# Optimization experiments

Hardware: AMD Instinct MI355X
Metric: run time of the kernel (lower is better)

Reference implementation:

```python
import jax, jax.numpy as jnp
import numpy as np

D = 128
N = 300000
M = 262144
LN_EPS = 1e-5


def setup_inputs() -> dict:
    key = jax.random.key(0)
    ks = jax.random.split(key, 20)
    inp = {
        'h_p': jax.random.normal(ks[0], (N, D), jnp.float32),
        'h_k': jax.random.normal(ks[1], (N, D), jnp.float32),
        'h_o': jax.random.normal(ks[2], (M, D), jnp.float32),
        'weight_o': jax.random.normal(ks[3], (D, D // 2), jnp.float32) * 0.15,
        'weight_p': jax.random.normal(ks[4], (D, D // 2), jnp.float32) * 0.15,
        'lin_W': jax.random.normal(ks[5], (D, D), jnp.float32) * 0.08,
        'lin_b': jax.random.normal(ks[6], (D,), jnp.float32) * 0.05,
        'bias': jax.random.normal(ks[7], (D,), jnp.float32) * 0.05,
        'Wq': jax.random.normal(ks[8], (D, D), jnp.float32) * 0.08,
        'bq': jax.random.normal(ks[9], (D,), jnp.float32) * 0.05,
        'Wk': jax.random.normal(ks[10], (D, D), jnp.float32) * 0.08,
        'bk': jax.random.normal(ks[11], (D,), jnp.float32) * 0.05,
        'Wv': jax.random.normal(ks[12], (D, D), jnp.float32) * 0.08,
        'bv': jax.random.normal(ks[13], (D,), jnp.float32) * 0.05,
        'W1': jax.random.normal(ks[14], (D, D), jnp.float32) * 0.08,
        'b1': jax.random.normal(ks[15], (D,), jnp.float32) * 0.05,
        'ln_g': jnp.ones((D,), jnp.float32),
        'ln_b': jnp.zeros((D,), jnp.float32),
        'mutual_index_p': jax.random.randint(ks[16], (M,), 0, N, jnp.int32),
        'mutual_index_k': jax.random.randint(ks[17], (M,), 0, N, jnp.int32),
        'propagation_node_num': N,
        'knowledge_node_num': N,
    }
    return inp


def reference(h_p, h_k, h_o, weight_o, weight_p, lin_W, lin_b, bias,
              Wq, bq, Wk, bk, Wv, bv, W1, b1, ln_g, ln_b,
              mutual_index_p, mutual_index_k,
              propagation_node_num, knowledge_node_num):
    # gather: Q from h_o rows, K from paired h_p/h_k rows (seq len 2)
    ho_sel = h_o[mutual_index_p]                       # [M, D]
    q = ho_sel[:, None, :]                             # [M, 1, D]
    k_in = jnp.stack([h_p[mutual_index_p], h_k[mutual_index_k]], axis=1)  # [M, 2, D]

    Q = q @ Wq.T + bq                                  # [M, 1, D]
    K = k_in @ Wk.T + bk                               # [M, 2, D]
    V = k_in @ Wv.T + bv                               # [M, 2, D]

    scale = jnp.float32(D) ** -0.5
    attn = jax.nn.softmax(jnp.einsum('mqd,mkd->mqk', Q, K) * scale, axis=-1)  # [M,1,2]
    ctx = jnp.einsum('mqk,mkd->mqd', attn, V)          # [M, 1, D]

    fusion = ctx @ W1.T + b1                           # dropout is identity in eval
    mu = jnp.mean(fusion, axis=-1, keepdims=True)
    var = jnp.var(fusion, axis=-1, keepdims=True)
    fusion = (fusion - mu) * jax.lax.rsqrt(var + LN_EPS) * ln_g + ln_b
    fusion = fusion[:, 0, :]                           # [M, D]

    trans_ho = ho_sel @ weight_o                       # [M, D/2]
    trans_pk = fusion @ weight_p                       # [M, D/2]
    out = jnp.tanh(jnp.concatenate([trans_ho, trans_pk], axis=1))
    out = jax.nn.leaky_relu(out @ lin_W.T + lin_b, negative_slope=0.01)
    out = out + bias                                   # [M, D]

    h_p = h_p.at[mutual_index_p].set(out)
    h_k = h_k.at[mutual_index_k].set(out)
    return (h_p, h_k)
```

## Files before the change

### kernel.cpp

```cpp
#include <hip/hip_runtime.h>
#include <stdint.h>

#define D 128
#define NROWS 300000
#define MIDX 262144
#define SBH 132
#define WAVE_BUF (16 * SBH)

typedef __attribute__((ext_vector_type(8))) short short8_t;
typedef __attribute__((ext_vector_type(4))) short short4_t;
typedef __attribute__((ext_vector_type(4))) float float4v;

__device__ __forceinline__ short f2bf(float x) {
  uint32_t u = __float_as_uint(x);
  u = (u + 0x7FFFu + ((u >> 16) & 1u)) >> 16;
  return (short)u;
}

__global__ void winners_kernel(const int* __restrict__ idx_p,
                               const int* __restrict__ idx_k,
                               int* __restrict__ wp, int* __restrict__ wk) {
  int m = blockIdx.x * 256 + threadIdx.x;
  if (m < MIDX) {
    atomicMax(&wp[idx_p[m]], m);
    atomicMax(&wk[idx_k[m]], m);
  }
}

__global__ __launch_bounds__(256)
void copyrest_kernel(const float* __restrict__ h_p, const float* __restrict__ h_k,
                     const int* __restrict__ wp, const int* __restrict__ wk,
                     float* __restrict__ out_p, float* __restrict__ out_k) {
  int g = blockIdx.x * 256 + threadIdx.x;
  int row = g >> 5;
  if (row >= NROWS) return;
  int c = (g & 31) << 2;
  size_t off = (size_t)row * D + c;
  if (wp[row] < 0) *(float4v*)(out_p + off) = *(const float4v*)(h_p + off);
  if (wk[row] < 0) *(float4v*)(out_k + off) = *(const float4v*)(h_k + off);
}

__global__ void pack_kernel(const float* __restrict__ Wq, const float* __restrict__ Wk,
                            const float* __restrict__ Wv, const float* __restrict__ W1,
                            const float* __restrict__ Wl, const float* __restrict__ Wo,
                            const float* __restrict__ Wp, short* __restrict__ dst) {
  int slot = blockIdx.x;
  int lane = threadIdx.x;
  const float* W; int base; int trans; int rel;
  if      (slot < 32)  { W = Wq; base = 0;     trans = 1; rel = slot; }
  else if (slot < 64)  { W = Wk; base = 16384; trans = 1; rel = slot - 32; }
  else if (slot < 96)  { W = Wv; base = 32768; trans = 1; rel = slot - 64; }
  else if (slot < 128) { W = W1; base = 49152; trans = 1; rel = slot - 96; }
  else if (slot < 160) { W = Wl; base = 65536; trans = 1; rel = slot - 128; }
  else if (slot < 176) { W = Wo; base = 81920; trans = 0; rel = slot - 160; }
  else                 { W = Wp; base = 90112; trans = 0; rel = slot - 176; }
  int t = rel >> 2, s = rel & 3;
  int n = 16 * t + (lane & 15);
  int kb = 32 * s + 8 * (lane >> 4);
  short* o = dst + base + (size_t)(rel * 64 + lane) * 8;
  #pragma unroll
  for (int j = 0; j < 8; j++) {
    float v = trans ? W[n * 128 + kb + j] : W[(kb + j) * 64 + n];
    o[j] = f2bf(v);
  }
}

__device__ __forceinline__ float4v gemm_tile_lds(const short8_t a[4], const short* B,
                                                 int t, int lane) {
  float4v acc = {0.f, 0.f, 0.f, 0.f};
  #pragma unroll
  for (int s = 0; s < 4; s++) {
    short8_t b = *(const short8_t*)(B + ((t * 4 + s) * 64 + lane) * 8);
    acc = __builtin_amdgcn_mfma_f32_16x16x32_bf16(a[s], b, acc, 0, 0, 0);
  }
  return acc;
}

__device__ __forceinline__ void load_row_frags(const float* __restrict__ row, int q, short8_t out[4]) {
  #pragma unroll
  for (int s = 0; s < 4; s++) {
    float4v v0 = *(const float4v*)(row + 32 * s + 8 * q);
    float4v v1 = *(const float4v*)(row + 32 * s + 8 * q + 4);
    short8_t r;
    r[0] = f2bf(v0[0]); r[1] = f2bf(v0[1]); r[2] = f2bf(v0[2]); r[3] = f2bf(v0[3]);
    r[4] = f2bf(v1[0]); r[5] = f2bf(v1[1]); r[6] = f2bf(v1[2]); r[7] = f2bf(v1[3]);
    out[s] = r;
  }
}

__device__ __forceinline__ void read_a_frags(const short* sb, int l15, int q, short8_t out[4]) {
  #pragma unroll
  for (int s = 0; s < 4; s++) {
    const short* p = sb + l15 * SBH + 32 * s + 8 * q;
    short4_t lo = *(const short4_t*)p;
    short4_t hi = *(const short4_t*)(p + 4);
    short8_t v;
    v[0] = lo[0]; v[1] = lo[1]; v[2] = lo[2]; v[3] = lo[3];
    v[4] = hi[0]; v[5] = hi[1]; v[6] = hi[2]; v[7] = hi[3];
    out[s] = v;
  }
}

__device__ __forceinline__ float red16(float v) {
  v += __shfl_xor(v, 1);
  v += __shfl_xor(v, 2);
  v += __shfl_xor(v, 4);
  v += __shfl_xor(v, 8);
  return v;
}

__global__ __launch_bounds__(256, 2)
void fused_kernel(const float* __restrict__ h_p, const float* __restrict__ h_k,
                  const float* __restrict__ h_o, int ho_rows,
                  const int* __restrict__ idx_p, const int* __restrict__ idx_k,
                  const short* __restrict__ wbuf,
                  const float* __restrict__ bq, const float* __restrict__ bk,
                  const float* __restrict__ bv, const float* __restrict__ b1,
                  const float* __restrict__ linb, const float* __restrict__ bias,
                  const float* __restrict__ lng, const float* __restrict__ lnb,
                  const int* __restrict__ wp, const int* __restrict__ wk,
                  float* __restrict__ out_p, float* __restrict__ out_k)
{
  const short* Bq_ = wbuf;
  const short* Bk_ = wbuf + 16384;
  const short* Bv_ = wbuf + 32768;
  const short* B1_ = wbuf + 49152;
  const short* Bl_ = wbuf + 65536;
  const short* Bo_ = wbuf + 81920;

  __shared__ short bsh[16384];
  __shared__ float smem[4 * WAVE_BUF];

  const int tid  = threadIdx.x;
  const int wave = tid >> 6;
  const int lane = tid & 63;
  const int l15  = lane & 15;
  const int q    = lane >> 4;

  float* fbuf = smem + wave * WAVE_BUF;
  short* sbuf = (short*)fbuf;

  const int m0   = blockIdx.x * 64 + wave * 16;
  const int mrow = m0 + l15;
  const int ip = idx_p[mrow];
  const int ik = idx_k[mrow];
  const int ipo = (ip < ho_rows) ? ip : (ho_rows - 1);

  short8_t aho[4], ahp[4], ahk[4];
  load_row_frags(h_o + (size_t)ipo * D, q, aho);
  load_row_frags(h_p + (size_t)ip * D, q, ahp);
  load_row_frags(h_k + (size_t)ik * D, q, ahk);

  short8_t breg[8];

  #define LDSTAGE(SRC) { _Pragma("unroll") \
    for (int r_ = 0; r_ < 8; r_++) breg[r_] = *(const short8_t*)((SRC) + (r_ * 256 + tid) * 8); }
  #define STSTAGE() { _Pragma("unroll") \
    for (int r_ = 0; r_ < 8; r_++) *(short8_t*)(bsh + (r_ * 256 + tid) * 8) = breg[r_]; }

  LDSTAGE(Bq_);
  STSTAGE();
  LDSTAGE(Bk_);
  __syncthreads();

  float4v Q[8];
  #pragma unroll
  for (int t = 0; t < 8; t++) {
    Q[t] = gemm_tile_lds(aho, bsh, t, lane) + bq[16 * t + l15];
  }

  __syncthreads();
  STSTAGE();
  LDSTAGE(Bv_);
  __syncthreads();

  float4v p0 = {0,0,0,0}, p1 = {0,0,0,0};
  #pragma unroll
  for (int t = 0; t < 8; t++) {
    float bkv = bk[16 * t + l15];
    float4v k0 = gemm_tile_lds(ahp, bsh, t, lane) + bkv;
    float4v k1 = gemm_tile_lds(ahk, bsh, t, lane) + bkv;
    p0 += Q[t] * k0;
    p1 += Q[t] * k1;
  }
  float a0[4], a1[4];
  #pragma unroll
  for (int r = 0; r < 4; r++) {
    float s0 = red16(p0[r]) * 0.08838834764831845f;
    float s1 = red16(p1[r]) * 0.08838834764831845f;
    float mx = fmaxf(s0, s1);
    float e0 = __expf(s0 - mx), e1 = __expf(s1 - mx);
    float inv = 1.0f / (e0 + e1);
    a0[r] = e0 * inv;
    a1[r] = e1 * inv;
  }

  __syncthreads();
  STSTAGE();
  LDSTAGE(B1_);
  __syncthreads();

  float4v ctx[8];
  #pragma unroll
  for (int t = 0; t < 8; t++) {
    float bvv = bv[16 * t + l15];
    float4v v0 = gemm_tile_lds(ahp, bsh, t, lane) + bvv;
    float4v v1 = gemm_tile_lds(ahk, bsh, t, lane) + bvv;
    float4v c;
    #pragma unroll
    for (int r = 0; r < 4; r++) c[r] = a0[r] * v0[r] + a1[r] * v1[r];
    ctx[t] = c;
  }

  #pragma unroll
  for (int t = 0; t < 8; t++)
    #pragma unroll
    for (int r = 0; r < 4; r++)
      sbuf[(4 * q + r) * SBH + 16 * t + l15] = f2bf(ctx[t][r]);
  short8_t afu[4];
  read_a_frags(sbuf, l15, q, afu);

  __syncthreads();
  STSTAGE();
  LDSTAGE(Bo_);
  __syncthreads();

  float4v F[8];
  float4v sum = {0,0,0,0}, ssq = {0,0,0,0};
  #pragma unroll
  for (int t = 0; t < 8; t++) {
    float4v f = gemm_tile_lds(afu, bsh, t, lane) + b1[16 * t + l15];
    F[t] = f;
    sum += f;
    ssq += f * f;
  }
  #pragma unroll
  for (int r = 0; r < 4; r++) {
    float s  = red16(sum[r]);
    float s2 = red16(ssq[r]);
    float mu  = s * (1.0f / 128.0f);
    float var = s2 * (1.0f / 128.0f) - mu * mu;
    float rs  = rsqrtf(var + 1e-5f);
    #pragma unroll
    for (int t = 0; t < 8; t++) F[t][r] = (F[t][r] - mu) * rs;
  }
  #pragma unroll
  for (int t = 0; t < 8; t++) {
    int col = 16 * t + l15;
    float g = lng[col], b = lnb[col];
    #pragma unroll
    for (int r = 0; r < 4; r++)
      sbuf[(4 * q + r) * SBH + col] = f2bf(F[t][r] * g + b);
  }
  short8_t afn[4];
  read_a_frags(sbuf, l15, q, afn);

  __syncthreads();
  STSTAGE();
  LDSTAGE(Bl_);
  __syncthreads();

  float4v U[8];
  #pragma unroll
  for (int t = 0; t < 4; t++) U[t]     = gemm_tile_lds(aho, bsh, t, lane);
  #pragma unroll
  for (int t = 0; t < 4; t++) U[4 + t] = gemm_tile_lds(afn, bsh + 8192, t, lane);
  #pragma unroll
  for (int t = 0; t < 8; t++) {
    #pragma unroll
    for (int r = 0; r < 4; r++) {
      float x  = U[t][r];
      float e  = __expf(-2.0f * fabsf(x));
      float th = (1.0f - e) / (1.0f + e);
      sbuf[(4 * q + r) * SBH + 16 * t + l15] = f2bf(copysignf(th, x));
    }
  }
  short8_t au[4];
  read_a_frags(sbuf, l15, q, au);

  __syncthreads();
  STSTAGE();
  __syncthreads();

  #pragma unroll
  for (int t = 0; t < 8; t++) {
    int col = 16 * t + l15;
    float4v z = gemm_tile_lds(au, bsh, t, lane) + linb[col];
    float bb = bias[col];
    #pragma unroll
    for (int r = 0; r < 4; r++) {
      float x = z[r];
      x = (x > 0.0f) ? x : 0.01f * x;
      fbuf[(4 * q + r) * SBH + col] = x + bb;
    }
  }

  int r_out = lane >> 2;
  int cb    = (lane & 3) * 32;
  int mg    = m0 + r_out;
  int ip2 = idx_p[mg];
  int ik2 = idx_k[mg];
  bool dop = (wp[ip2] == mg);
  bool dok = (wk[ik2] == mg);
  const float* src = fbuf + r_out * SBH + cb;
  float* dp = out_p + (size_t)ip2 * D + cb;
  float* dk = out_k + (size_t)ik2 * D + cb;
  #pragma unroll
  for (int c = 0; c < 32; c += 4) {
    float4v v = *(const float4v*)(src + c);
    if (dop) *(float4v*)(dp + c) = v;
    if (dok) *(float4v*)(dk + c) = v;
  }
  #undef LDSTAGE
  #undef STSTAGE
}

extern "C" void kernel_launch(void* const* d_in, const int* in_sizes, int n_in,
                              void* d_out, int out_size, void* d_ws, size_t ws_size,
                              hipStream_t stream) {
  const float* h_p      = (const float*)d_in[0];
  const float* h_k      = (const float*)d_in[1];
  const float* h_o      = (const float*)d_in[2];
  const float* weight_o = (const float*)d_in[3];
  const float* weight_p = (const float*)d_in[4];
  const float* lin_W    = (const float*)d_in[5];
  const float* lin_b    = (const float*)d_in[6];
  const float* bias     = (const float*)d_in[7];
  const float* Wq       = (const float*)d_in[8];
  const float* bq       = (const float*)d_in[9];
  const float* Wk       = (const float*)d_in[10];
  const float* bk       = (const float*)d_in[11];
  const float* Wv       = (const float*)d_in[12];
  const float* bv       = (const float*)d_in[13];
  const float* W1       = (const float*)d_in[14];
  const float* b1       = (const float*)d_in[15];
  const float* ln_g     = (const float*)d_in[16];
  const float* ln_b     = (const float*)d_in[17];
  const int*   idx_p    = (const int*)d_in[18];
  const int*   idx_k    = (const int*)d_in[19];

  const int ho_rows = in_sizes[2] / D;

  float* out_p = (float*)d_out;
  float* out_k = out_p + (size_t)NROWS * D;

  int* wp = (int*)d_ws;
  int* wk = wp + NROWS;
  short* wbuf = (short*)((char*)d_ws + (size_t)2 * NROWS * 4);

  hipMemsetAsync(wp, 0xFF, (size_t)2 * NROWS * sizeof(int), stream);

  winners_kernel<<<dim3(MIDX / 256), dim3(256), 0, stream>>>(idx_p, idx_k, wp, wk);
  copyrest_kernel<<<dim3((NROWS * 32 + 255) / 256), dim3(256), 0, stream>>>(
      h_p, h_k, wp, wk, out_p, out_k);
  pack_kernel<<<dim3(192), dim3(64), 0, stream>>>(Wq, Wk, Wv, W1, lin_W, weight_o, weight_p, wbuf);
  fused_kernel<<<dim3(MIDX / 64), dim3(256), 0, stream>>>(
      h_p, h_k, h_o, ho_rows, idx_p, idx_k, wbuf, bq, bk, bv, b1, lin_b, bias, ln_g, ln_b,
      wp, wk, out_p, out_k);
}
```

Baseline: 763.0 us.

## Fold Wq and Wk into one matrix and process two row tiles per wave

Measured after the change: 750.9 us. No clear change (-1.6%).

```diff
diff --git a/kernel.cpp b/kernel.cpp
--- a/kernel.cpp
+++ b/kernel.cpp
@@ -5,7 +5,7 @@
 #define NROWS 300000
 #define MIDX 262144
 #define SBH 132
-#define WAVE_BUF (16 * SBH)
+#define WBUF_SH (32 * SBH)
 
 typedef __attribute__((ext_vector_type(8))) short short8_t;
 typedef __attribute__((ext_vector_type(4))) short short4_t;
@@ -15,6 +15,9 @@
   uint32_t u = __float_as_uint(x);
   u = (u + 0x7FFFu + ((u >> 16) & 1u)) >> 16;
   return (short)u;
+}
+__device__ __forceinline__ float bf2f(short s) {
+  return __uint_as_float(((uint32_t)(uint16_t)s) << 16);
 }
 
 __global__ void winners_kernel(const int* __restrict__ idx_p,
@@ -40,40 +43,70 @@
   if (wk[row] < 0) *(float4v*)(out_k + off) = *(const float4v*)(h_k + off);
 }
 
-__global__ void pack_kernel(const float* __restrict__ Wq, const float* __restrict__ Wk,
-                            const float* __restrict__ Wv, const float* __restrict__ W1,
-                            const float* __restrict__ Wl, const float* __restrict__ Wo,
-                            const float* __restrict__ Wp, short* __restrict__ dst) {
+__global__ void prep_m_kernel(const float* __restrict__ Wq, const float* __restrict__ Wk,
+                              const float* __restrict__ bq,
+                              float* __restrict__ Mbuf, float* __restrict__ v2) {
+  int b = blockIdx.x;
+  if (b < 64) {
+    int d = ((b >> 3) << 4) + (threadIdx.x >> 4);
+    int e = ((b & 7) << 4) + (threadIdx.x & 15);
+    float acc = 0.f;
+    for (int j = 0; j < 128; j++) acc += Wq[j * 128 + d] * Wk[j * 128 + e];
+    Mbuf[d * 128 + e] = acc;
+  } else if (threadIdx.x < 128) {
+    int e = threadIdx.x;
+    float acc = 0.f;
+    for (int j = 0; j < 128; j++) acc += bq[j] * Wk[j * 128 + e];
+    v2[e] = acc;
+  }
+}
+
+__global__ void pack_kernel(const float* __restrict__ Mb, const float* __restrict__ Wv,
+                            const float* __restrict__ W1, const float* __restrict__ Wl,
+                            const float* __restrict__ Wo, const float* __restrict__ Wp,
+                            short* __restrict__ dst) {
   int slot = blockIdx.x;
   int lane = threadIdx.x;
-  const float* W; int base; int trans; int rel;
-  if      (slot < 32)  { W = Wq; base = 0;     trans = 1; rel = slot; }
-  else if (slot < 64)  { W = Wk; base = 16384; trans = 1; rel = slot - 32; }
-  else if (slot < 96)  { W = Wv; base = 32768; trans = 1; rel = slot - 64; }
-  else if (slot < 128) { W = W1; base = 49152; trans = 1; rel = slot - 96; }
-  else if (slot < 160) { W = Wl; base = 65536; trans = 1; rel = slot - 128; }
-  else if (slot < 176) { W = Wo; base = 81920; trans = 0; rel = slot - 160; }
-  else                 { W = Wp; base = 90112; trans = 0; rel = slot - 176; }
+  const float* W; int base; int trans; int rel; int wdt = 128;
+  if      (slot < 32)  { W = Mb; base = 0;     trans = 0; rel = slot; }
+  else if (slot < 64)  { W = Wv; base = 16384; trans = 1; rel = slot - 32; }
+  else if (slot < 96)  { W = W1; base = 32768; trans = 1; rel = slot - 64; }
+  else if (slot < 112) { W = Wo; base = 49152; trans = 0; rel = slot - 96;  wdt = 64; }
+  else if (slot < 128) { W = Wp; base = 57344; trans = 0; rel = slot - 112; wdt = 64; }
+  else                 { W = Wl; base = 65536; trans = 1; rel = slot - 128; }
   int t = rel >> 2, s = rel & 3;
   int n = 16 * t + (lane & 15);
   int kb = 32 * s + 8 * (lane >> 4);
   short* o = dst + base + (size_t)(rel * 64 + lane) * 8;
   #pragma unroll
   for (int j = 0; j < 8; j++) {
-    float v = trans ? W[n * 128 + kb + j] : W[(kb + j) * 64 + n];
+    float v = trans ? W[n * 128 + kb + j] : W[(kb + j) * wdt + n];
     o[j] = f2bf(v);
   }
 }
 
-__device__ __forceinline__ float4v gemm_tile_lds(const short8_t a[4], const short* B,
-                                                 int t, int lane) {
-  float4v acc = {0.f, 0.f, 0.f, 0.f};
+__device__ __forceinline__ void gemm2(const short8_t a0[4], const short8_t a1[4],
+                                      const short* B, int t, int lane,
+                                      float4v& c0, float4v& c1) {
   #pragma unroll
   for (int s = 0; s < 4; s++) {
     short8_t b = *(const short8_t*)(B + ((t * 4 + s) * 64 + lane) * 8);
-    acc = __builtin_amdgcn_mfma_f32_16x16x32_bf16(a[s], b, acc, 0, 0, 0);
-  }
-  return acc;
+    c0 = __builtin_amdgcn_mfma_f32_16x16x32_bf16(a0[s], b, c0, 0, 0, 0);
+    c1 = __builtin_amdgcn_mfma_f32_16x16x32_bf16(a1[s], b, c1, 0, 0, 0);
+  }
+}
+__device__ __forceinline__ void gemm4(const short8_t a0[4], const short8_t a1[4],
+                                      const short8_t a2[4], const short8_t a3[4],
+                                      const short* B, int t, int lane,
+                                      float4v& c0, float4v& c1, float4v& c2, float4v& c3) {
+  #pragma unroll
+  for (int s = 0; s < 4; s++) {
+    short8_t b = *(const short8_t*)(B + ((t * 4 + s) * 64 + lane) * 8);
+    c0 = __builtin_amdgcn_mfma_f32_16x16x32_bf16(a0[s], b, c0, 0, 0, 0);
+    c1 = __builtin_amdgcn_mfma_f32_16x16x32_bf16(a1[s], b, c1, 0, 0, 0);
+    c2 = __builtin_amdgcn_mfma_f32_16x16x32_bf16(a2[s], b, c2, 0, 0, 0);
+    c3 = __builtin_amdgcn_mfma_f32_16x16x32_bf16(a3[s], b, c3, 0, 0, 0);
+  }
 }
 
 __device__ __forceinline__ void load_row_frags(const float* __restrict__ row, int q, short8_t out[4]) {
@@ -88,10 +121,10 @@
   }
 }
 
-__device__ __forceinline__ void read_a_frags(const short* sb, int l15, int q, short8_t out[4]) {
+__device__ __forceinline__ void read_a_frags(const short* sb, int row, int q, short8_t out[4]) {
   #pragma unroll
   for (int s = 0; s < 4; s++) {
-    const short* p = sb + l15 * SBH + 32 * s + 8 * q;
+    const short* p = sb + row * SBH + 32 * s + 8 * q;
     short4_t lo = *(const short4_t*)p;
     short4_t hi = *(const short4_t*)(p + 4);
     short8_t v;
@@ -113,23 +146,21 @@
 void fused_kernel(const float* __restrict__ h_p, const float* __restrict__ h_k,
                   const float* __restrict__ h_o, int ho_rows,
                   const int* __restrict__ idx_p, const int* __restrict__ idx_k,
-                  const short* __restrict__ wbuf,
-                  const float* __restrict__ bq, const float* __restrict__ bk,
+                  const short* __restrict__ wbuf, const float* __restrict__ v2,
                   const float* __restrict__ bv, const float* __restrict__ b1,
                   const float* __restrict__ linb, const float* __restrict__ bias,
                   const float* __restrict__ lng, const float* __restrict__ lnb,
                   const int* __restrict__ wp, const int* __restrict__ wk,
                   float* __restrict__ out_p, float* __restrict__ out_k)
 {
-  const short* Bq_ = wbuf;
-  const short* Bk_ = wbuf + 16384;
-  const short* Bv_ = wbuf + 32768;
-  const short* B1_ = wbuf + 49152;
-  const short* Bl_ = wbuf + 65536;
-  const short* Bo_ = wbuf + 81920;
+  const short* Bm_  = wbuf;
+  const short* Bv_  = wbuf + 16384;
+  const short* B1_  = wbuf + 32768;
+  const short* Bop_ = wbuf + 49152;
+  const short* Bl_  = wbuf + 65536;
 
   __shared__ short bsh[16384];
-  __shared__ float smem[4 * WAVE_BUF];
+  __shared__ short tmem[4 * WBUF_SH];
 
   const int tid  = threadIdx.x;
   const int wave = tid >> 6;
@@ -137,19 +168,24 @@
   const int l15  = lane & 15;
   const int q    = lane >> 4;
 
-  float* fbuf = smem + wave * WAVE_BUF;
-  short* sbuf = (short*)fbuf;
-
-  const int m0   = blockIdx.x * 64 + wave * 16;
-  const int mrow = m0 + l15;
-  const int ip = idx_p[mrow];
-  const int ik = idx_k[mrow];
-  const int ipo = (ip < ho_rows) ? ip : (ho_rows - 1);
-
-  short8_t aho[4], ahp[4], ahk[4];
-  load_row_frags(h_o + (size_t)ipo * D, q, aho);
-  load_row_frags(h_p + (size_t)ip * D, q, ahp);
-  load_row_frags(h_k + (size_t)ik * D, q, ahk);
+  short* sbuf = tmem + wave * WBUF_SH;
+  float* fbuf = (float*)sbuf;
+
+  const int m0  = blockIdx.x * 128 + wave * 32;
+  const int mr0 = m0 + l15;
+  const int mr1 = m0 + 16 + l15;
+  const int ip0 = idx_p[mr0], ik0 = idx_k[mr0];
+  const int ip1 = idx_p[mr1], ik1 = idx_k[mr1];
+  const int ipo0 = (ip0 < ho_rows) ? ip0 : (ho_rows - 1);
+  const int ipo1 = (ip1 < ho_rows) ? ip1 : (ho_rows - 1);
+
+  short8_t aho0[4], ahp0[4], ahk0[4], aho1[4], ahp1[4], ahk1[4];
+  load_row_frags(h_o + (size_t)ipo0 * D, q, aho0);
+  load_row_frags(h_p + (size_t)ip0 * D, q, ahp0);
+  load_row_frags(h_k + (size_t)ik0 * D, q, ahk0);
+  load_row_frags(h_o + (size_t)ipo1 * D, q, aho1);
+  load_row_frags(h_p + (size_t)ip1 * D, q, ahp1);
+  load_row_frags(h_k + (size_t)ik1 * D, q, ahk1);
 
   short8_t breg[8];
 
@@ -158,41 +194,57 @@
   #define STSTAGE() { _Pragma("unroll") \
     for (int r_ = 0; r_ < 8; r_++) *(short8_t*)(bsh + (r_ * 256 + tid) * 8) = breg[r_]; }
 
-  LDSTAGE(Bq_);
-  STSTAGE();
-  LDSTAGE(Bk_);
-  __syncthreads();
-
-  float4v Q[8];
-  #pragma unroll
-  for (int t = 0; t < 8; t++) {
-    Q[t] = gemm_tile_lds(aho, bsh, t, lane) + bq[16 * t + l15];
-  }
-
-  __syncthreads();
+  LDSTAGE(Bm_);
   STSTAGE();
   LDSTAGE(Bv_);
   __syncthreads();
 
-  float4v p0 = {0,0,0,0}, p1 = {0,0,0,0};
-  #pragma unroll
-  for (int t = 0; t < 8; t++) {
-    float bkv = bk[16 * t + l15];
-    float4v k0 = gemm_tile_lds(ahp, bsh, t, lane) + bkv;
-    float4v k1 = gemm_tile_lds(ahk, bsh, t, lane) + bkv;
-    p0 += Q[t] * k0;
-    p1 += Q[t] * k1;
-  }
-  float a0[4], a1[4];
+  #pragma unroll
+  for (int t = 0; t < 8; t++) {
+    float4v g0 = {0,0,0,0}, g1 = {0,0,0,0};
+    gemm2(aho0, aho1, bsh, t, lane, g0, g1);
+    float vv = v2[16 * t + l15];
+    #pragma unroll
+    for (int r = 0; r < 4; r++) {
+      sbuf[(4 * q + r) * SBH + 16 * t + l15]        = f2bf(g0[r] + vv);
+      sbuf[(16 + 4 * q + r) * SBH + 16 * t + l15]   = f2bf(g1[r] + vv);
+    }
+  }
+  short8_t afg0[4], afg1[4];
+  read_a_frags(sbuf, l15, q, afg0);
+  read_a_frags(sbuf, 16 + l15, q, afg1);
+
+  float e00 = 0.f, e01 = 0.f, e10 = 0.f, e11 = 0.f;
+  #pragma unroll
+  for (int s = 0; s < 4; s++)
+    #pragma unroll
+    for (int j = 0; j < 8; j++) {
+      float ga = bf2f(afg0[s][j]);
+      float gb = bf2f(afg1[s][j]);
+      e00 += ga * bf2f(ahp0[s][j]);
+      e01 += ga * bf2f(ahk0[s][j]);
+      e10 += gb * bf2f(ahp1[s][j]);
+      e11 += gb * bf2f(ahk1[s][j]);
+    }
+  e00 += __shfl_xor(e00, 16); e00 += __shfl_xor(e00, 32);
+  e01 += __shfl_xor(e01, 16); e01 += __shfl_xor(e01, 32);
+  e10 += __shfl_xor(e10, 16); e10 += __shfl_xor(e10, 32);
+  e11 += __shfl_xor(e11, 16); e11 += __shfl_xor(e11, 32);
+  const float sc = 0.08838834764831845f;
+  float s00 = e00 * sc, s01 = e01 * sc, s10 = e10 * sc, s11 = e11 * sc;
+  float mx0 = fmaxf(s00, s01), mx1 = fmaxf(s10, s11);
+  float x00 = __expf(s00 - mx0), x01 = __expf(s01 - mx0);
+  float x10 = __expf(s10 - mx1), x11 = __expf(s11 - mx1);
+  float i0 = 1.0f / (x00 + x01), i1 = 1.0f / (x10 + x11);
+  float w00 = x00 * i0, w01 = x01 * i0, w10 = x10 * i1, w11 = x11 * i1;
+  float a00[4], a01[4], a10[4], a11[4];
   #pragma unroll
   for (int r = 0; r < 4; r++) {
-    float s0 = red16(p0[r]) * 0.08838834764831845f;
-    float s1 = red16(p1[r]) * 0.08838834764831845f;
-    float mx = fmaxf(s0, s1);
-    float e0 = __expf(s0 - mx), e1 = __expf(s1 - mx);
-    float inv = 1.0f / (e0 + e1);
-    a0[r] = e0 * inv;
-    a1[r] = e1 * inv;
+    int src = 4 * q + r;
+    a00[r] = __shfl(w00, src);
+    a01[r] = __shfl(w01, src);
+    a10[r] = __shfl(w10, src);
+    a11[r] = __shfl(w11, src);
   }
 
   __syncthreads();
@@ -200,116 +252,163 @@
   LDSTAGE(B1_);
   __syncthreads();
 
-  float4v ctx[8];
-  #pragma unroll
-  for (int t = 0; t < 8; t++) {
+  #pragma unroll
+  for (int t = 0; t < 8; t++) {
+    float4v vp0 = {0,0,0,0}, vk0 = {0,0,0,0}, vp1 = {0,0,0,0}, vk1 = {0,0,0,0};
+    gemm4(ahp0, ahk0, ahp1, ahk1, bsh, t, lane, vp0, vk0, vp1, vk1);
     float bvv = bv[16 * t + l15];
-    float4v v0 = gemm_tile_lds(ahp, bsh, t, lane) + bvv;
-    float4v v1 = gemm_tile_lds(ahk, bsh, t, lane) + bvv;
-    float4v c;
-    #pragma unroll
-    for (int r = 0; r < 4; r++) c[r] = a0[r] * v0[r] + a1[r] * v1[r];
-    ctx[t] = c;
-  }
-
-  #pragma unroll
-  for (int t = 0; t < 8; t++)
-    #pragma unroll
-    for (int r = 0; r < 4; r++)
-      sbuf[(4 * q + r) * SBH + 16 * t + l15] = f2bf(ctx[t][r]);
-  short8_t afu[4];
-  read_a_frags(sbuf, l15, q, afu);
+    #pragma unroll
+    for (int r = 0; r < 4; r++) {
+      float c0 = a00[r] * (vp0[r] + bvv) + a01[r] * (vk0[r] + bvv);
+      float c1 = a10[r] * (vp1[r] + bvv) + a11[r] * (vk1[r] + bvv);
+      sbuf[(4 * q + r) * SBH + 16 * t + l15]      = f2bf(c0);
+      sbuf[(16 + 4 * q + r) * SBH + 16 * t + l15] = f2bf(c1);
+    }
+  }
+  short8_t afu0[4], afu1[4];
+  read_a_frags(sbuf, l15, q, afu0);
+  read_a_frags(sbuf, 16 + l15, q, afu1);
 
   __syncthreads();
   STSTAGE();
-  LDSTAGE(Bo_);
-  __syncthreads();
-
-  float4v F[8];
-  float4v sum = {0,0,0,0}, ssq = {0,0,0,0};
-  #pragma unroll
-  for (int t = 0; t < 8; t++) {
-    float4v f = gemm_tile_lds(afu, bsh, t, lane) + b1[16 * t + l15];
-    F[t] = f;
-    sum += f;
-    ssq += f * f;
-  }
+  LDSTAGE(Bop_);
+  __syncthreads();
+
+  float4v F0[8], F1[8];
+  float4v sum0 = {0,0,0,0}, ssq0 = {0,0,0,0}, sum1 = {0,0,0,0}, ssq1 = {0,0,0,0};
+  #pragma unroll
+  for (int t = 0; t < 8; t++) {
+    float4v f0 = {0,0,0,0}, f1 = {0,0,0,0};
+    gemm2(afu0, afu1, bsh, t, lane, f0, f1);
+    float bb = b1[16 * t + l15];
+    f0 = f0 + bb; f1 = f1 + bb;
+    F0[t] = f0; F1[t] = f1;
+    sum0 += f0; ssq0 += f0 * f0;
+    sum1 += f1; ssq1 += f1 * f1;
+  }
+  float mu0[4], rs0[4], mu1[4], rs1[4];
   #pragma unroll
   for (int r = 0; r < 4; r++) {
-    float s  = red16(sum[r]);
-    float s2 = red16(ssq[r]);
-    float mu  = s * (1.0f / 128.0f);
-    float var = s2 * (1.0f / 128.0f) - mu * mu;
-    float rs  = rsqrtf(var + 1e-5f);
-    #pragma unroll
-    for (int t = 0; t < 8; t++) F[t][r] = (F[t][r] - mu) * rs;
+    float s  = red16(sum0[r]);
+    float s2 = red16(ssq0[r]);
+    float m  = s * (1.0f / 128.0f);
+    mu0[r] = m;
+    rs0[r] = rsqrtf(s2 * (1.0f / 128.0f) - m * m + 1e-5f);
+    s  = red16(sum1[r]);
+    s2 = red16(ssq1[r]);
+    m  = s * (1.0f / 128.0f);
+    mu1[r] = m;
+    rs1[r] = rsqrtf(s2 * (1.0f / 128.0f) - m * m + 1e-5f);
   }
   #pragma unroll
   for (int t = 0; t < 8; t++) {
     int col = 16 * t + l15;
     float g = lng[col], b = lnb[col];
     #pragma unroll
-    for (int r = 0; r < 4; r++)
-      sbuf[(4 * q + r) * SBH + col] = f2bf(F[t][r] * g + b);
-  }
-  short8_t afn[4];
-  read_a_frags(sbuf, l15, q, afn);
+    for (int r = 0; r < 4; r++) {
+      sbuf[(4 * q + r) * SBH + col]      = f2bf((F0[t][r] - mu0[r]) * rs0[r] * g + b);
+      sbuf[(16 + 4 * q + r) * SBH + col] = f2bf((F1[t][r] - mu1[r]) * rs1[r] * g + b);
+    }
+  }
+  short8_t afn0[4], afn1[4];
+  read_a_frags(sbuf, l15, q, afn0);
+  read_a_frags(sbuf, 16 + l15, q, afn1);
 
   __syncthreads();
   STSTAGE();
   LDSTAGE(Bl_);
   __syncthreads();
 
-  float4v U[8];
-  #pragma unroll
-  for (int t = 0; t < 4; t++) U[t]     = gemm_tile_lds(aho, bsh, t, lane);
-  #pragma unroll
-  for (int t = 0; t < 4; t++) U[4 + t] = gemm_tile_lds(afn, bsh + 8192, t, lane);
-  #pragma unroll
-  for (int t = 0; t < 8; t++) {
-    #pragma unroll
-    for (int r = 0; r < 4; r++) {
-      float x  = U[t][r];
-      float e  = __expf(-2.0f * fabsf(x));
-      float th = (1.0f - e) / (1.0f + e);
-      sbuf[(4 * q + r) * SBH + 16 * t + l15] = f2bf(copysignf(th, x));
-    }
-  }
-  short8_t au[4];
-  read_a_frags(sbuf, l15, q, au);
+  #pragma unroll
+  for (int t = 0; t < 4; t++) {
+    float4v u0 = {0,0,0,0}, u1 = {0,0,0,0};
+    gemm2(aho0, aho1, bsh, t, lane, u0, u1);
+    #pragma unroll
+    for (int r = 0; r < 4; r++) {
+      float xa = u0[r], ea = __expf(-2.0f * fabsf(xa));
+      float xb = u1[r], eb = __expf(-2.0f * fabsf(xb));
+      sbuf[(4 * q + r) * SBH + 16 * t + l15]      = f2bf(copysignf((1.0f - ea) / (1.0f + ea), xa));
+      sbuf[(16 + 4 * q + r) * SBH + 16 * t + l15] = f2bf(copysignf((1.0f - eb) / (1.0f + eb), xb));
+    }
+  }
+  #pragma unroll
+  for (int t = 0; t < 4; t++) {
+    float4v u0 = {0,0,0,0}, u1 = {0,0,0,0};
+    gemm2(afn0, afn1, bsh + 8192, t, lane, u0, u1);
+    #pragma unroll
+    for (int r = 0; r < 4; r++) {
+      float xa = u0[r], ea = __expf(-2.0f * fabsf(xa));
+      float xb = u1[r], eb = __expf(-2.0f * fabsf(xb));
+      sbuf[(4 * q + r) * SBH + 64 + 16 * t + l15]      = f2bf(copysignf((1.0f - ea) / (1.0f + ea), xa));
+      sbuf[(16 + 4 * q + r) * SBH + 64 + 16 * t + l15] = f2bf(copysignf((1.0f - eb) / (1.0f + eb), xb));
+    }
+  }
+  short8_t au0[4], au1[4];
+  read_a_frags(sbuf, l15, q, au0);
+  read_a_frags(sbuf, 16 + l15, q, au1);
 
   __syncthreads();
   STSTAGE();
   __syncthreads();
 
+  float4v z0[8], z1[8];
+  #pragma unroll
+  for (int t = 0; t < 8; t++) {
+    float4v c0 = {0,0,0,0}, c1 = {0,0,0,0};
+    gemm2(au0, au1, bsh, t, lane, c0, c1);
+    float lb = linb[16 * t + l15];
+    z0[t] = c0 + lb;
+    z1[t] = c1 + lb;
+  }
   #pragma unroll
   for (int t = 0; t < 8; t++) {
     int col = 16 * t + l15;
-    float4v z = gemm_tile_lds(au, bsh, t, lane) + linb[col];
     float bb = bias[col];
     #pragma unroll
     for (int r = 0; r < 4; r++) {
-      float x = z[r];
+      float x = z0[t][r];
       x = (x > 0.0f) ? x : 0.01f * x;
       fbuf[(4 * q + r) * SBH + col] = x + bb;
     }
   }
-
-  int r_out = lane >> 2;
-  int cb    = (lane & 3) * 32;
-  int mg    = m0 + r_out;
-  int ip2 = idx_p[mg];
-  int ik2 = idx_k[mg];
-  bool dop = (wp[ip2] == mg);
-  bool dok = (wk[ik2] == mg);
-  const float* src = fbuf + r_out * SBH + cb;
-  float* dp = out_p + (size_t)ip2 * D + cb;
-  float* dk = out_k + (size_t)ik2 * D + cb;
-  #pragma unroll
-  for (int c = 0; c < 32; c += 4) {
-    float4v v = *(const float4v*)(src + c);
-    if (dop) *(float4v*)(dp + c) = v;
-    if (dok) *(float4v*)(dk + c) = v;
+  {
+    int r_out = lane >> 2, cb = (lane & 3) * 32, mg = m0 + r_out;
+    int ip2 = idx_p[mg], ik2 = idx_k[mg];
+    bool dop = (wp[ip2] == mg), dok = (wk[ik2] == mg);
+    const float* src = fbuf + r_out * SBH + cb;
+    float* dp = out_p + (size_t)ip2 * D + cb;
+    float* dk = out_k + (size_t)ik2 * D + cb;
+    #pragma unroll
+    for (int c = 0; c < 32; c += 4) {
+      float4v v = *(const float4v*)(src + c);
+      if (dop) *(float4v*)(dp + c) = v;
+      if (dok) *(float4v*)(dk + c) = v;
+    }
+  }
+  #pragma unroll
+  for (int t = 0; t < 8; t++) {
+    int col = 16 * t + l15;
+    float bb = bias[col];
+    #pragma unroll
+    for (int r = 0; r < 4; r++) {
+      float x = z1[t][r];
+      x = (x > 0.0f) ? x : 0.01f * x;
+      fbuf[(4 * q + r) * SBH + col] = x + bb;
+    }
+  }
+  {
+    int r_out = lane >> 2, cb = (lane & 3) * 32, mg = m0 + 16 + r_out;
+    int ip2 = idx_p[mg], ik2 = idx_k[mg];
+    bool dop = (wp[ip2] == mg), dok = (wk[ik2] == mg);
+    const float* src = fbuf + r_out * SBH + cb;
+    float* dp = out_p + (size_t)ip2 * D + cb;
+    float* dk = out_k + (size_t)ik2 * D + cb;
+    #pragma unroll
+    for (int c = 0; c < 32; c += 4) {
+      float4v v = *(const float4v*)(src + c);
+      if (dop) *(float4v*)(dp + c) = v;
+      if (dok) *(float4v*)(dk + c) = v;
+    }
   }
   #undef LDSTAGE
   #undef STSTAGE
@@ -338,6 +437,7 @@
   const float* ln_b     = (const float*)d_in[17];
   const int*   idx_p    = (const int*)d_in[18];
   const int*   idx_k    = (const int*)d_in[19];
+  (void)bk;
 
   const int ho_rows = in_sizes[2] / D;
 
@@ -347,14 +447,17 @@
   int* wp = (int*)d_ws;
   int* wk = wp + NROWS;
   short* wbuf = (short*)((char*)d_ws + (size_t)2 * NROWS * 4);
+  float* Mbuf = (float*)((char*)wbuf + 81920 * 2);
+  float* v2   = Mbuf + 128 * 128;
 
   hipMemsetAsync(wp, 0xFF, (size_t)2 * NROWS * sizeof(int), stream);
 
   winners_kernel<<<dim3(MIDX / 256), dim3(256), 0, stream>>>(idx_p, idx_k, wp, wk);
   copyrest_kernel<<<dim3((NROWS * 32 + 255) / 256), dim3(256), 0, stream>>>(
       h_p, h_k, wp, wk, out_p, out_k);
-  pack_kernel<<<dim3(192), dim3(64), 0, stream>>>(Wq, Wk, Wv, W1, lin_W, weight_o, weight_p, wbuf);
-  fused_kernel<<<dim3(MIDX / 64), dim3(256), 0, stream>>>(
-      h_p, h_k, h_o, ho_rows, idx_p, idx_k, wbuf, bq, bk, bv, b1, lin_b, bias, ln_g, ln_b,
+  prep_m_kernel<<<dim3(65), dim3(256), 0, stream>>>(Wq, Wk, bq, Mbuf, v2);
+  pack_kernel<<<dim3(160), dim3(64), 0, stream>>>(Mbuf, Wv, W1, lin_W, weight_o, weight_p, wbuf);
+  fused_kernel<<<dim3(MIDX / 128), dim3(256), 0, stream>>>(
+      h_p, h_k, h_o, ho_rows, idx_p, idx_k, wbuf, v2, bv, b1, lin_b, bias, ln_g, ln_b,
       wp, wk, out_p, out_k);
 }
```
